# Kernel tuning notes

Measured on AMD Instinct MI355X. Metric: run time of the kernel, lower is better.

Reference implementation:

```python
import jax, jax.numpy as jnp
import numpy as np

N, E, D, H, K = 8192, 8, 1024, 4096, 2


def setup_inputs() -> dict:
    key = jax.random.key(0)
    ks = jax.random.split(key, 12)
    s = 0.02  # init scale for weights
    return {
        "x": jax.random.normal(ks[0], (N, D), jnp.float32),
        "noise": jax.random.normal(ks[1], (N, E), jnp.float32),
        "Wg_w": jax.random.normal(ks[2], (D, E), jnp.float32) * s,
        "Wg_b": jnp.zeros((E,), jnp.float32),
        "Wn_w": jax.random.normal(ks[3], (D, E), jnp.float32) * s,
        "Wn_b": jnp.zeros((E,), jnp.float32),
        "w1": jax.random.normal(ks[4], (E, D, H), jnp.float32) * s,
        "b1": jnp.zeros((E, H), jnp.float32),
        "w2": jax.random.normal(ks[5], (E, H, D), jnp.float32) * s,
        "b2": jnp.zeros((E, D), jnp.float32),
        "k": K,
    }


def reference(x, noise, Wg_w, Wg_b, Wn_w, Wn_b, w1, b1, w2, b2, k):
    # --- noisy top-k gating: H(x) = Wg(x) + noise * softplus(Wn(x)) ---
    g_logits = x @ Wg_w + Wg_b                       # [N, E]
    n_scale = jax.nn.softplus(x @ Wn_w + Wn_b)       # [N, E]
    h = g_logits + noise * n_scale                   # [N, E]
    topk_vals, topk_inds = jax.lax.top_k(h, k)       # [N, k]
    gates = jax.nn.softmax(topk_vals, axis=-1)       # [N, k]

    # Scatter top-k gates into a dense [N, E] map (zeros for unselected experts),
    # so the weighted combine is exactly sum_j gates[n,j] * expert_{inds[n,j]}(x_n).
    n_tok, n_exp = h.shape
    dense_gates = jnp.zeros((n_tok, n_exp), h.dtype).at[
        jnp.arange(n_tok)[:, None], topk_inds
    ].set(gates)                                     # [N, E]

    # --- per-expert 2-layer MLP: fc2(relu(fc1(x))) ---
    hid = jax.nn.relu(jnp.einsum('nd,edh->neh', x, w1) + b1)  # [N, E, H]
    y = jnp.einsum('neh,ehd->ned', hid, w2) + b2              # [N, E, D]
    out = jnp.einsum('ned,ne->nd', y, dense_gates)            # [N, D]
    return out
```

## Files before the change

### kernel.cpp

```cpp
#include <hip/hip_runtime.h>
#include <hip/hip_bf16.h>

#define NTOK 8192
#define NEXP 8
#define DMODEL 1024
#define DHID 4096

typedef __bf16 bf16x8 __attribute__((ext_vector_type(8)));
typedef float f32x4 __attribute__((ext_vector_type(4)));

__device__ __forceinline__ unsigned short f2bf(float f) {
  return __builtin_bit_cast(unsigned short, __float2bfloat16(f));
}

__device__ __forceinline__ void gload_lds16(const void* g, void* l) {
  __builtin_amdgcn_global_load_lds(
      (const __attribute__((address_space(1))) unsigned int*)g,
      (__attribute__((address_space(3))) unsigned int*)l, 16, 0, 0);
}

__device__ __forceinline__ int imin(int a, int b) { return a < b ? a : b; }

constexpr size_t OFF_XB   = 0;
constexpr size_t OFF_W1T  = OFF_XB + (size_t)NTOK * DMODEL * 2;
constexpr size_t OFF_W2T  = OFF_W1T + (size_t)NEXP * DHID * DMODEL * 2;
constexpr size_t OFF_HID  = OFF_W2T + (size_t)NEXP * DMODEL * DHID * 2;
constexpr size_t OFF_IDX  = OFF_HID + (size_t)NTOK * 2 * DHID * 2;
constexpr size_t OFF_GATE = OFF_IDX + (size_t)NTOK * 2 * 4;
constexpr size_t OFF_LIST = OFF_GATE + (size_t)NTOK * 2 * 4;
constexpr size_t OFF_CNT  = OFF_LIST + (size_t)NTOK * 2 * 4;
constexpr size_t OFF_OFFS = OFF_CNT + 128;
constexpr size_t OFF_CUR  = OFF_OFFS + 128;

__global__ void transpose_bf16_kernel(const float* __restrict__ in,
                                      unsigned short* __restrict__ out,
                                      int R, int C) {
  __shared__ float sh[64][65];
  const size_t ebase = (size_t)blockIdx.z * R * C;
  const float* ine = in + ebase;
  unsigned short* oute = out + ebase;
  int c0 = blockIdx.x * 64, r0 = blockIdx.y * 64;
  int tx = threadIdx.x & 15, ty = threadIdx.x >> 4;
#pragma unroll
  for (int p = 0; p < 4; ++p) {
    int row = ty + p * 16;
    float4 v = *(const float4*)&ine[(size_t)(r0 + row) * C + c0 + tx * 4];
    sh[row][tx * 4 + 0] = v.x;
    sh[row][tx * 4 + 1] = v.y;
    sh[row][tx * 4 + 2] = v.z;
    sh[row][tx * 4 + 3] = v.w;
  }
  __syncthreads();
#pragma unroll
  for (int p = 0; p < 4; ++p) {
    int crow = ty + p * 16;
    ushort4 o;
    o.x = f2bf(sh[tx * 4 + 0][crow]);
    o.y = f2bf(sh[tx * 4 + 1][crow]);
    o.z = f2bf(sh[tx * 4 + 2][crow]);
    o.w = f2bf(sh[tx * 4 + 3][crow]);
    *(ushort4*)&oute[(size_t)(c0 + crow) * R + r0 + tx * 4] = o;
  }
}

__global__ void gating_kernel(const float* __restrict__ x,
                              const float* __restrict__ noise,
                              const float* __restrict__ Wg_w,
                              const float* __restrict__ Wg_b,
                              const float* __restrict__ Wn_w,
                              const float* __restrict__ Wn_b,
                              unsigned short* __restrict__ xb,
                              int* __restrict__ topk_idx,
                              float* __restrict__ topk_gate,
                              int* __restrict__ counts) {
  int wave = threadIdx.x >> 6;
  int lane = threadIdx.x & 63;
  int n = blockIdx.x * 4 + wave;
  if (n >= NTOK) return;

  float ag[8] = {0.f, 0.f, 0.f, 0.f, 0.f, 0.f, 0.f, 0.f};
  float an[8] = {0.f, 0.f, 0.f, 0.f, 0.f, 0.f, 0.f, 0.f};
  const float* xr = x + (size_t)n * DMODEL;
  unsigned short* xbr = xb + (size_t)n * DMODEL;
#pragma unroll 4
  for (int i = 0; i < DMODEL / 64; ++i) {
    int d = lane + i * 64;
    float xv = xr[d];
    xbr[d] = f2bf(xv);
    const float4* wg = (const float4*)(Wg_w + (size_t)d * 8);
    const float4* wn = (const float4*)(Wn_w + (size_t)d * 8);
    float4 g0 = wg[0], g1 = wg[1];
    float4 n0 = wn[0], n1 = wn[1];
    ag[0] += xv * g0.x; ag[1] += xv * g0.y; ag[2] += xv * g0.z; ag[3] += xv * g0.w;
    ag[4] += xv * g1.x; ag[5] += xv * g1.y; ag[6] += xv * g1.z; ag[7] += xv * g1.w;
    an[0] += xv * n0.x; an[1] += xv * n0.y; an[2] += xv * n0.z; an[3] += xv * n0.w;
    an[4] += xv * n1.x; an[5] += xv * n1.y; an[6] += xv * n1.z; an[7] += xv * n1.w;
  }
#pragma unroll
  for (int off = 32; off > 0; off >>= 1) {
#pragma unroll
    for (int j = 0; j < 8; ++j) {
      ag[j] += __shfl_down(ag[j], off, 64);
      an[j] += __shfl_down(an[j], off, 64);
    }
  }
  if (lane == 0) {
    float h[8];
#pragma unroll
    for (int e = 0; e < 8; ++e) {
      float gl = ag[e] + Wg_b[e];
      float z = an[e] + Wn_b[e];
      float sp = fmaxf(z, 0.f) + log1pf(expf(-fabsf(z)));
      h[e] = gl + noise[(size_t)n * 8 + e] * sp;
    }
    int i0 = 0; float v0 = h[0];
#pragma unroll
    for (int e = 1; e < 8; ++e)
      if (h[e] > v0) { v0 = h[e]; i0 = e; }
    int i1 = -1; float v1 = -1e30f;
#pragma unroll
    for (int e = 0; e < 8; ++e)
      if (e != i0 && h[e] > v1) { v1 = h[e]; i1 = e; }
    float e1 = expf(v1 - v0);
    float inv = 1.f / (1.f + e1);
    topk_idx[n * 2] = i0;
    topk_idx[n * 2 + 1] = i1;
    topk_gate[n * 2] = inv;
    topk_gate[n * 2 + 1] = e1 * inv;
    atomicAdd(&counts[i0], 1);
    atomicAdd(&counts[i1], 1);
  }
}

__global__ void scan_kernel(const int* __restrict__ counts,
                            int* __restrict__ offsets, int* __restrict__ cursor) {
  if (threadIdx.x == 0) {
    int acc = 0;
    for (int e = 0; e < NEXP; ++e) {
      offsets[e] = acc;
      cursor[e] = acc;
      acc += counts[e];
    }
    offsets[NEXP] = acc;
  }
}

__global__ void scatter_kernel(const int* __restrict__ topk_idx,
                               int* __restrict__ cursor, int* __restrict__ list) {
  int n = blockIdx.x * 256 + threadIdx.x;
  if (n >= NTOK) return;
#pragma unroll
  for (int j = 0; j < 2; ++j) {
    int e = topk_idx[n * 2 + j];
    int pos = atomicAdd(&cursor[e], 1);
    list[pos] = n * 2 + j;
  }
}

template <int MODE>
__global__ __launch_bounds__(512, 2) void expert_gemm(
    const unsigned short* __restrict__ Asrc, const unsigned short* __restrict__ Bt,
    const float* __restrict__ bias, const int* __restrict__ offsets,
    const int* __restrict__ list, const float* __restrict__ gates,
    unsigned short* __restrict__ hid, float* __restrict__ out) {
  constexpr int K = MODE ? DHID : DMODEL;
  constexpr int Nout = MODE ? DMODEL : DHID;
  constexpr int NT = K / 64;

  const int gx = gridDim.x, gy = gridDim.y;
  const int lin = blockIdx.x + gx * (blockIdx.y + gy * blockIdx.z);
  const int e = lin & 7;
  const int r = lin >> 3;
  const int by = r % gy;
  const int bx = r / gy;

  const int off = offsets[e];
  const int ne = offsets[e + 1] - off;
  const int m0 = by * 256;
  if (m0 >= ne) return;
  const int n0 = bx * 256;

  __shared__ alignas(16) unsigned short Al[2][256 * 64];
  __shared__ alignas(16) unsigned short Bl[2][256 * 64];

  const int tid = threadIdx.x;
  const int lane = tid & 63;
  const int w = tid >> 6;
  const int wMi = w >> 2;
  const int wNi = w & 3;
  const int lr = lane & 15;
  const int kg = lane >> 4;
  const int cxor = (lr & 7) * 8;

  const unsigned short* a_src[4];
  const unsigned short* b_src[4];
#pragma unroll
  for (int i = 0; i < 4; ++i) {
    int L = tid + i * 512;
    int row = L >> 3, c = L & 7;
    int cs = c ^ (row & 7);
    int p = off + imin(m0 + row, ne - 1);
    if (MODE == 0) {
      int token = list[p] >> 1;
      a_src[i] = Asrc + (size_t)token * DMODEL + cs * 8;
    } else {
      a_src[i] = Asrc + (size_t)p * DHID + cs * 8;
    }
    b_src[i] = Bt + (size_t)e * Nout * K + (size_t)(n0 + row) * K + cs * 8;
  }

  f32x4 acc[8][4] = {};

  auto stage = [&](int buf, int kt) {
#pragma unroll
    for (int i = 0; i < 4; ++i)
      gload_lds16(a_src[i] + kt * 64, &Al[buf][(tid + i * 512) * 8]);
#pragma unroll
    for (int i = 0; i < 4; ++i)
      gload_lds16(b_src[i] + kt * 64, &Bl[buf][(tid + i * 512) * 8]);
  };

  auto compute = [&](int buf) {
#pragma unroll
    for (int kk = 0; kk < 2; ++kk) {
      const int ch = ((kk * 4 + kg) * 8) ^ cxor;
      bf16x8 bfr[4], af[8];
#pragma unroll
      for (int nf = 0; nf < 4; ++nf) {
        int rr = wNi * 64 + nf * 16 + lr;
        bfr[nf] = *(const bf16x8*)&Bl[buf][rr * 64 + ch];
      }
#pragma unroll
      for (int mf = 0; mf < 8; ++mf) {
        int rr = wMi * 128 + mf * 16 + lr;
        af[mf] = *(const bf16x8*)&Al[buf][rr * 64 + ch];
      }
#pragma unroll
      for (int mf = 0; mf < 8; ++mf)
#pragma unroll
        for (int nf = 0; nf < 4; ++nf)
          acc[mf][nf] = __builtin_amdgcn_mfma_f32_16x16x32_bf16(af[mf], bfr[nf],
                                                                acc[mf][nf], 0, 0, 0);
    }
  };

  stage(0, 0);
  int cur = 0;
  for (int t = 0; t < NT; ++t) {
    if (t + 1 < NT) {
      stage(cur ^ 1, t + 1);
      asm volatile("s_waitcnt vmcnt(8)" ::: "memory");
    } else {
      asm volatile("s_waitcnt vmcnt(0)" ::: "memory");
    }
    __builtin_amdgcn_s_barrier();
    compute(cur);
    asm volatile("s_waitcnt lgkmcnt(0)" ::: "memory");
    __builtin_amdgcn_sched_barrier(0);
    __builtin_amdgcn_s_barrier();
    cur ^= 1;
  }

  if (MODE == 0) {
#pragma unroll
    for (int mf = 0; mf < 8; ++mf) {
#pragma unroll
      for (int j = 0; j < 4; ++j) {
        int rloc = wMi * 128 + mf * 16 + kg * 4 + j;
        int row = m0 + rloc;
        if (row < ne) {
          size_t p = (size_t)(off + row);
#pragma unroll
          for (int nf = 0; nf < 4; ++nf) {
            int col = n0 + wNi * 64 + nf * 16 + lr;
            float v = acc[mf][nf][j] + bias[(size_t)e * Nout + col];
            hid[p * DHID + col] = f2bf(fmaxf(v, 0.f));
          }
        }
      }
    }
  } else {
#pragma unroll
    for (int mf = 0; mf < 8; ++mf) {
#pragma unroll
      for (int j = 0; j < 4; ++j) {
        int rloc = wMi * 128 + mf * 16 + kg * 4 + j;
        int row = m0 + rloc;
        if (row < ne) {
          int lv = list[off + row];
          int token = lv >> 1;
          float g = gates[lv];
#pragma unroll
          for (int nf = 0; nf < 4; ++nf) {
            int col = n0 + wNi * 64 + nf * 16 + lr;
            float v = (acc[mf][nf][j] + bias[(size_t)e * Nout + col]) * g;
            atomicAdd(&out[(size_t)token * DMODEL + col], v);
          }
        }
      }
    }
  }
}

extern "C" void kernel_launch(void* const* d_in, const int* in_sizes, int n_in,
                              void* d_out, int out_size, void* d_ws, size_t ws_size,
                              hipStream_t stream) {
  const float* x = (const float*)d_in[0];
  const float* noise = (const float*)d_in[1];
  const float* Wg_w = (const float*)d_in[2];
  const float* Wg_b = (const float*)d_in[3];
  const float* Wn_w = (const float*)d_in[4];
  const float* Wn_b = (const float*)d_in[5];
  const float* w1 = (const float*)d_in[6];
  const float* b1 = (const float*)d_in[7];
  const float* w2 = (const float*)d_in[8];
  const float* b2 = (const float*)d_in[9];
  float* out = (float*)d_out;

  char* ws = (char*)d_ws;
  unsigned short* xb = (unsigned short*)(ws + OFF_XB);
  unsigned short* w1t = (unsigned short*)(ws + OFF_W1T);
  unsigned short* w2t = (unsigned short*)(ws + OFF_W2T);
  unsigned short* hid = (unsigned short*)(ws + OFF_HID);
  int* topk_idx = (int*)(ws + OFF_IDX);
  float* topk_gate = (float*)(ws + OFF_GATE);
  int* list = (int*)(ws + OFF_LIST);
  int* counts = (int*)(ws + OFF_CNT);
  int* offsets = (int*)(ws + OFF_OFFS);
  int* cursor = (int*)(ws + OFF_CUR);

  hipMemsetAsync(out, 0, (size_t)NTOK * DMODEL * sizeof(float), stream);
  hipMemsetAsync(counts, 0, NEXP * sizeof(int), stream);

  transpose_bf16_kernel<<<dim3(DHID / 64, DMODEL / 64, NEXP), 256, 0, stream>>>(
      w1, w1t, DMODEL, DHID);
  transpose_bf16_kernel<<<dim3(DMODEL / 64, DHID / 64, NEXP), 256, 0, stream>>>(
      w2, w2t, DHID, DMODEL);

  gating_kernel<<<NTOK / 4, 256, 0, stream>>>(x, noise, Wg_w, Wg_b, Wn_w, Wn_b,
                                              xb, topk_idx, topk_gate, counts);
  scan_kernel<<<1, 64, 0, stream>>>(counts, offsets, cursor);
  scatter_kernel<<<NTOK / 256, 256, 0, stream>>>(topk_idx, cursor, list);

  expert_gemm<0><<<dim3(DHID / 256, 32, NEXP), 512, 0, stream>>>(
      xb, w1t, b1, offsets, list, topk_gate, hid, nullptr);
  expert_gemm<1><<<dim3(DMODEL / 256, 32, NEXP), 512, 0, stream>>>(
      hid, w2t, b2, offsets, list, topk_gate, nullptr, out);
}
```

Baseline: 1.014 ms.

## Interleave global-to-LDS prefetch with MFMA phases in expert GEMM main loop

Restructures the expert GEMM K-loop into four phases. Each phase issues a slice of the next tile's global-to-LDS loads, reads a subset of A/B fragments from LDS, and runs 16 MFMAs at raised wave priority. The goal is to overlap memory loads with matrix math and to cut register pressure by holding 4 A fragments instead of 8. It also precomputes the swizzled LDS offsets, hardcodes 64 row-blocks per expert (up from 32) so imbalanced routing is covered, and adds barriers between phases, which could cost extra sync overhead.

```diff
diff --git a/kernel.cpp b/kernel.cpp
--- a/kernel.cpp
+++ b/kernel.cpp
@@ -157,6 +157,26 @@
   }
 }
 
+#define STAGE_A(SLOT, KTN, I) gload_lds16(a_src[I] + (size_t)(KTN) * 64, &Al[SLOT][dstOff[I]])
+#define STAGE_B(SLOT, KTN, I) gload_lds16(b_src[I] + (size_t)(KTN) * 64, &Bl[SLOT][dstOff[I]])
+#define LDS_A(MB, CHK)                                                  \
+  _Pragma("unroll") for (int m_ = 0; m_ < 4; ++m_)                      \
+      af[m_] = *(const bf16x8*)(aCur + ((MB) + m_) * 1024 + (CHK));
+#define LDS_B(CHK)                                                      \
+  _Pragma("unroll") for (int n_ = 0; n_ < 4; ++n_)                      \
+      bfr[n_] = *(const bf16x8*)(bCur + n_ * 1024 + (CHK));
+#define MFMA16(MB)                                                      \
+  __builtin_amdgcn_s_setprio(1);                                        \
+  _Pragma("unroll") for (int nf_ = 0; nf_ < 4; ++nf_) {                 \
+    _Pragma("unroll") for (int m_ = 0; m_ < 4; ++m_)                    \
+        acc[(MB) + m_][nf_] = __builtin_amdgcn_mfma_f32_16x16x32_bf16(  \
+            af[m_], bfr[nf_], acc[(MB) + m_][nf_], 0, 0, 0);            \
+  }                                                                     \
+  __builtin_amdgcn_s_setprio(0);
+#define WAIT_LGKM0()                                      \
+  asm volatile("s_waitcnt lgkmcnt(0)" ::: "memory");      \
+  __builtin_amdgcn_sched_barrier(0);
+
 template <int MODE>
 __global__ __launch_bounds__(512, 2) void expert_gemm(
     const unsigned short* __restrict__ Asrc, const unsigned short* __restrict__ Bt,
@@ -167,12 +187,12 @@
   constexpr int Nout = MODE ? DMODEL : DHID;
   constexpr int NT = K / 64;
 
-  const int gx = gridDim.x, gy = gridDim.y;
-  const int lin = blockIdx.x + gx * (blockIdx.y + gy * blockIdx.z);
+  const int gx = gridDim.x;
+  const int lin = blockIdx.x + gx * (blockIdx.y + 64 * blockIdx.z);
   const int e = lin & 7;
   const int r = lin >> 3;
-  const int by = r % gy;
-  const int bx = r / gy;
+  const int by = r & 63;
+  const int bx = r >> 6;
 
   const int off = offsets[e];
   const int ne = offsets[e + 1] - off;
@@ -190,15 +210,19 @@
   const int wNi = w & 3;
   const int lr = lane & 15;
   const int kg = lane >> 4;
-  const int cxor = (lr & 7) * 8;
+
+  const int chk0 = ((kg ^ (lr & 7)) * 8);
+  const int chk1 = (((4 + kg) ^ (lr & 7)) * 8);
 
   const unsigned short* a_src[4];
   const unsigned short* b_src[4];
+  int dstOff[4];
 #pragma unroll
   for (int i = 0; i < 4; ++i) {
     int L = tid + i * 512;
     int row = L >> 3, c = L & 7;
     int cs = c ^ (row & 7);
+    dstOff[i] = L * 8;
     int p = off + imin(m0 + row, ne - 1);
     if (MODE == 0) {
       int token = list[p] >> 1;
@@ -210,55 +234,48 @@
   }
 
   f32x4 acc[8][4] = {};
-
-  auto stage = [&](int buf, int kt) {
-#pragma unroll
-    for (int i = 0; i < 4; ++i)
-      gload_lds16(a_src[i] + kt * 64, &Al[buf][(tid + i * 512) * 8]);
-#pragma unroll
-    for (int i = 0; i < 4; ++i)
-      gload_lds16(b_src[i] + kt * 64, &Bl[buf][(tid + i * 512) * 8]);
-  };
-
-  auto compute = [&](int buf) {
-#pragma unroll
-    for (int kk = 0; kk < 2; ++kk) {
-      const int ch = ((kk * 4 + kg) * 8) ^ cxor;
-      bf16x8 bfr[4], af[8];
-#pragma unroll
-      for (int nf = 0; nf < 4; ++nf) {
-        int rr = wNi * 64 + nf * 16 + lr;
-        bfr[nf] = *(const bf16x8*)&Bl[buf][rr * 64 + ch];
-      }
-#pragma unroll
-      for (int mf = 0; mf < 8; ++mf) {
-        int rr = wMi * 128 + mf * 16 + lr;
-        af[mf] = *(const bf16x8*)&Al[buf][rr * 64 + ch];
-      }
-#pragma unroll
-      for (int mf = 0; mf < 8; ++mf)
-#pragma unroll
-        for (int nf = 0; nf < 4; ++nf)
-          acc[mf][nf] = __builtin_amdgcn_mfma_f32_16x16x32_bf16(af[mf], bfr[nf],
-                                                                acc[mf][nf], 0, 0, 0);
-    }
-  };
-
-  stage(0, 0);
-  int cur = 0;
-  for (int t = 0; t < NT; ++t) {
-    if (t + 1 < NT) {
-      stage(cur ^ 1, t + 1);
-      asm volatile("s_waitcnt vmcnt(8)" ::: "memory");
+  bf16x8 af[4], bfr[4];
+
+#pragma unroll
+  for (int i = 0; i < 4; ++i) { STAGE_A(0, 0, i); STAGE_B(0, 0, i); }
+
+  for (int kt = 0; kt < NT; ++kt) {
+    const int s = kt & 1;
+    const int ns = s ^ 1;
+    const bool pf = (kt + 1 < NT);
+    const unsigned short* aCur = &Al[s][(wMi * 128 + lr) * 64];
+    const unsigned short* bCur = &Bl[s][(wNi * 64 + lr) * 64];
+
+    if (pf) {
+      STAGE_A(ns, kt + 1, 0); STAGE_A(ns, kt + 1, 1);
+      asm volatile("s_waitcnt vmcnt(2)" ::: "memory");
     } else {
       asm volatile("s_waitcnt vmcnt(0)" ::: "memory");
     }
     __builtin_amdgcn_s_barrier();
-    compute(cur);
-    asm volatile("s_waitcnt lgkmcnt(0)" ::: "memory");
     __builtin_amdgcn_sched_barrier(0);
-    __builtin_amdgcn_s_barrier();
-    cur ^= 1;
+    LDS_A(0, chk0) LDS_B(chk0)
+    WAIT_LGKM0()
+    MFMA16(0)
+    __builtin_amdgcn_s_barrier();
+
+    LDS_A(4, chk0)
+    if (pf) { STAGE_A(ns, kt + 1, 2); STAGE_A(ns, kt + 1, 3); }
+    WAIT_LGKM0()
+    MFMA16(4)
+    __builtin_amdgcn_s_barrier();
+
+    LDS_A(0, chk1) LDS_B(chk1)
+    if (pf) { STAGE_B(ns, kt + 1, 0); STAGE_B(ns, kt + 1, 1); }
+    WAIT_LGKM0()
+    MFMA16(0)
+    __builtin_amdgcn_s_barrier();
+
+    LDS_A(4, chk1)
+    if (pf) { STAGE_B(ns, kt + 1, 2); STAGE_B(ns, kt + 1, 3); }
+    WAIT_LGKM0()
+    MFMA16(4)
+    __builtin_amdgcn_s_barrier();
   }
 
   if (MODE == 0) {
@@ -342,8 +359,8 @@
   scan_kernel<<<1, 64, 0, stream>>>(counts, offsets, cursor);
   scatter_kernel<<<NTOK / 256, 256, 0, stream>>>(topk_idx, cursor, list);
 
-  expert_gemm<0><<<dim3(DHID / 256, 32, NEXP), 512, 0, stream>>>(
+  expert_gemm<0><<<dim3(DHID / 256, 64, NEXP), 512, 0, stream>>>(
       xb, w1t, b1, offsets, list, topk_gate, hid, nullptr);
-  expert_gemm<1><<<dim3(DMODEL / 256, 32, NEXP), 512, 0, stream>>>(
+  expert_gemm<1><<<dim3(DMODEL / 256, 64, NEXP), 512, 0, stream>>>(
       hid, w2t, b2, offsets, list, topk_gate, nullptr, out);
 }
```

New measurement: 994.1 us. 2.0% less time.
